# Performance work log

Hardware: AMD Instinct MI355X
Metric: run time of the kernel (lower is better)

Reference implementation:

```python
import jax, jax.numpy as jnp
import numpy as np

NEG = jnp.float32(-1e9)


def setup_inputs() -> dict:
    key = jax.random.key(0)
    ks = jax.random.split(key, 8)
    B, S, D = 8, 2048, 1024
    scale = 1.0 / np.sqrt(D)
    return {
        "xQ": jax.random.normal(ks[0], (B, S, D), jnp.float32),
        "xK": jax.random.normal(ks[1], (B, S, D), jnp.float32),
        "xV": jax.random.normal(ks[2], (B, S, D), jnp.float32),
        "padding_mask": jax.random.randint(ks[3], (B, S), 0, 2, jnp.int32),
        "casual_mask": jnp.ones((B, S), jnp.int32),
        "W_q": jax.random.normal(ks[4], (D, D), jnp.float32) * scale,
        "b_q": jnp.zeros((D,), jnp.float32),
        "W_k": jax.random.normal(ks[5], (D, D), jnp.float32) * scale,
        "b_k": jnp.zeros((D,), jnp.float32),
        "W_v": jax.random.normal(ks[6], (D, D), jnp.float32) * scale,
        "b_v": jnp.zeros((D,), jnp.float32),
    }


def reference(xQ, xK, xV, padding_mask, casual_mask, W_q, b_q, W_k, b_k, W_v, b_v):
    # Linear projections (torch nn.Linear: x @ W.T + b)
    Q = jnp.einsum('bsd,ed->bse', xQ, W_q) + b_q
    K = jnp.einsum('bsd,ed->bse', xK, W_k) + b_k
    V = jnp.einsum('bsd,ed->bse', xV, W_v) + b_v

    # Raw logits (note: original code applies NO 1/sqrt(dk) scaling)
    QKT = jnp.einsum('bqd,bkd->bqk', Q, K)  # [B, Sq, Sk]

    # Additive padding mask: -1e9 on padded key positions
    pad = jnp.where(padding_mask[:, None, :] == 0, NEG, jnp.float32(0.0))
    # Additive causal mask: -1e9 above the diagonal
    Sq, Sk = QKT.shape[1], QKT.shape[2]
    caus = jnp.where(
        jnp.tril(jnp.ones((Sq, Sk), dtype=bool)), jnp.float32(0.0), NEG
    )[None, :, :]
    QKT = QKT + pad + caus

    S = jax.nn.softmax(QKT, axis=-1)
    return jnp.einsum('bqk,bkd->bqd', S, V)
```

## Files before the change

### kernel.cpp

```cpp
#include <hip/hip_runtime.h>

typedef __attribute__((ext_vector_type(4))) float f4;
typedef __attribute__((ext_vector_type(4))) float f32x4;
typedef _Float16 half8 __attribute__((ext_vector_type(8)));

#define DEVI static __device__ __forceinline__

DEVI void gload_lds16(const void* g, void* l) {
  __builtin_amdgcn_global_load_lds(
      (const __attribute__((address_space(1))) void*)g,
      (__attribute__((address_space(3))) void*)l, 16, 0, 0);
}

DEVI int xcd_swz(int id, int n) {
  int q = n >> 3, r = n & 7;
  int x = id & 7, c = id >> 3;
  return (x < r ? x * (q + 1) : r * (q + 1) + (x - r) * q) + c;
}

#define FENCED_BARRIER()                \
  __builtin_amdgcn_sched_barrier(0);    \
  __builtin_amdgcn_s_barrier();         \
  __builtin_amdgcn_sched_barrier(0);

#define SWZ(kgv, rowv) ((((kgv) ^ ((rowv) >> 1)) & 3) * 8)

__global__ __launch_bounds__(256) void cvt_plain(const float* __restrict__ X,
                                                 _Float16* __restrict__ H,
                                                 int n4) {
  int i = blockIdx.x * 256 + threadIdx.x;
  const int stride = gridDim.x * 256;
  typedef _Float16 half4v __attribute__((ext_vector_type(4)));
  for (; i < n4; i += stride) {
    f4 x = ((const f4*)X)[i];
    half4v h;
#pragma unroll
    for (int j = 0; j < 4; ++j) h[j] = (_Float16)x[j];
    ((half4v*)H)[i] = h;
  }
}

__global__ __launch_bounds__(256) void cvt_split(const float* __restrict__ X,
                                                 _Float16* __restrict__ H,
                                                 _Float16* __restrict__ L,
                                                 int n4) {
  int i = blockIdx.x * 256 + threadIdx.x;
  const int stride = gridDim.x * 256;
  typedef _Float16 half4v __attribute__((ext_vector_type(4)));
  for (; i < n4; i += stride) {
    f4 x = ((const f4*)X)[i];
    half4v h, l;
#pragma unroll
    for (int j = 0; j < 4; ++j) {
      h[j] = (_Float16)x[j];
      l[j] = (_Float16)(x[j] - (float)h[j]);
    }
    ((half4v*)H)[i] = h;
    ((half4v*)L)[i] = l;
  }
}

DEVI void acc_zero44(f32x4 (&acc)[4][4]) {
#pragma unroll
  for (int i = 0; i < 4; ++i)
#pragma unroll
    for (int j = 0; j < 4; ++j) acc[i][j] = (f32x4)0.0f;
}
DEVI void acc_zero42(f32x4 (&acc)[4][2]) {
#pragma unroll
  for (int i = 0; i < 4; ++i)
#pragma unroll
    for (int j = 0; j < 2; ++j) acc[i][j] = (f32x4)0.0f;
}

template <int WSPLIT, int OUTMODE>
__global__ __launch_bounds__(512, 4) void proj3(
    const _Float16* __restrict__ X, const _Float16* __restrict__ Wh,
    const _Float16* __restrict__ Wl, const float* __restrict__ bias,
    _Float16* __restrict__ OutHi, _Float16* __restrict__ OutLo,
    _Float16* __restrict__ VtOut) {
  extern __shared__ _Float16 lds[];
  constexpr int ACH = 128 * 32;
  constexpr int BCH = 128 * 32;
  constexpr int CHUNK = ACH + BCH * (1 + WSPLIT);
  const int id = xcd_swz(blockIdx.x, gridDim.x);
  const int m0 = (id >> 3) * 128, n0 = (id & 7) * 128;
  const _Float16* A0 = X + (size_t)m0 * 1024;
  const _Float16* B0 = Wh + (size_t)n0 * 1024;
  const _Float16* B1 = Wl + (size_t)n0 * 1024;
  const int tid = threadIdx.x;
  const int w = tid >> 6, lane = tid & 63;
  const int wm = w >> 2, wn = w & 3;
  const int r16 = lane & 15, kg = lane >> 4;
  f32x4 acc[4][2];
  acc_zero42(acc);

  auto STAGE = [&](int t, int buf) {
    _Float16* base = lds + buf * CHUNK;
    int row = tid >> 2, c = tid & 3;
    int cs = (c ^ (row >> 1)) & 3;
    size_t src = (size_t)row * 1024 + t * 32 + cs * 8;
    gload_lds16(A0 + src, base + tid * 8);
    gload_lds16(B0 + src, base + ACH + tid * 8);
    if (WSPLIT) gload_lds16(B1 + src, base + ACH + BCH + tid * 8);
  };
  auto COMPUTE = [&](int buf) {
    const _Float16* la = lds + buf * CHUNK;
    const _Float16* lb = la + ACH;
    half8 a[4], b0f[2], b1f[2];
#pragma unroll
    for (int mi = 0; mi < 4; ++mi) {
      int row = wm * 64 + mi * 16 + r16;
      a[mi] = *(const half8*)(la + row * 32 + SWZ(kg, row));
    }
#pragma unroll
    for (int ni = 0; ni < 2; ++ni) {
      int row = wn * 32 + ni * 16 + r16;
      int off = row * 32 + SWZ(kg, row);
      b0f[ni] = *(const half8*)(lb + off);
      if (WSPLIT) b1f[ni] = *(const half8*)(lb + BCH + off);
    }
    __builtin_amdgcn_s_setprio(1);
#pragma unroll
    for (int mi = 0; mi < 4; ++mi)
#pragma unroll
      for (int ni = 0; ni < 2; ++ni) {
        acc[mi][ni] = __builtin_amdgcn_mfma_f32_16x16x32_f16(
            a[mi], b0f[ni], acc[mi][ni], 0, 0, 0);
        if (WSPLIT)
          acc[mi][ni] = __builtin_amdgcn_mfma_f32_16x16x32_f16(
              a[mi], b1f[ni], acc[mi][ni], 0, 0, 0);
      }
    __builtin_amdgcn_s_setprio(0);
  };

  const int NS = 32;
  STAGE(0, 0);
  STAGE(1, 1);
  int tt = 0;
  for (; tt < NS - 1; ++tt) {
    if constexpr (WSPLIT)
      asm volatile("s_waitcnt vmcnt(3)" ::: "memory");
    else
      asm volatile("s_waitcnt vmcnt(2)" ::: "memory");
    FENCED_BARRIER();
    if (tt + 2 < NS) STAGE(tt + 2, (tt + 2) % 3);
    COMPUTE(tt % 3);
  }
  asm volatile("s_waitcnt vmcnt(0)" ::: "memory");
  FENCED_BARRIER();
  COMPUTE(tt % 3);

  float bcol[2];
#pragma unroll
  for (int ni = 0; ni < 2; ++ni) bcol[ni] = bias[n0 + wn * 32 + ni * 16 + r16];

  if (OUTMODE != 2) {
#pragma unroll
    for (int mi = 0; mi < 4; ++mi) {
      int row = m0 + wm * 64 + mi * 16 + kg * 4;
#pragma unroll
      for (int ni = 0; ni < 2; ++ni) {
        int col = n0 + wn * 32 + ni * 16 + r16;
#pragma unroll
        for (int j = 0; j < 4; ++j) {
          float v = acc[mi][ni][j] + bcol[ni];
          _Float16 h = (_Float16)v;
          OutHi[(size_t)(row + j) * 1024 + col] = h;
          if (OUTMODE == 0)
            OutLo[(size_t)(row + j) * 1024 + col] = (_Float16)(v - (float)h);
        }
      }
    }
  } else {
    __syncthreads();
    _Float16(*T)[128] = (_Float16(*)[128])lds;
#pragma unroll
    for (int mi = 0; mi < 4; ++mi) {
      int ml = wm * 64 + mi * 16 + kg * 4;
#pragma unroll
      for (int ni = 0; ni < 2; ++ni) {
        int nl = wn * 32 + ni * 16 + r16;
#pragma unroll
        for (int j = 0; j < 4; ++j)
          T[nl][ml + j] = (_Float16)(acc[mi][ni][j] + bcol[ni]);
      }
    }
    __syncthreads();
    const int b = m0 >> 11;
    const int s0 = m0 & 2047;
#pragma unroll
    for (int r = 0; r < 4; ++r) {
      int flat = tid + r * 512;
      int n = flat >> 4, c = flat & 15;
      half8 v = *(const half8*)&T[n][c * 8];
      *(half8*)(VtOut + (size_t)b * (1024 * 2048) + (size_t)(n0 + n) * 2048 +
                s0 + c * 8) = v;
    }
  }
}

template <int WSPLIT, int OUTMODE>
__global__ __launch_bounds__(512, 2) void proj_fused(
    const float* __restrict__ X, const _Float16* __restrict__ Wh,
    const _Float16* __restrict__ Wl, const float* __restrict__ bias,
    _Float16* __restrict__ OutHi, _Float16* __restrict__ OutLo,
    _Float16* __restrict__ VtOut) {
  extern __shared__ _Float16 lds[];
  constexpr int ACH = 256 * 32;
  constexpr int BCH = 128 * 32;
  constexpr int CHUNK = ACH + BCH * (1 + WSPLIT);
  const int id = xcd_swz(blockIdx.x, gridDim.x);
  const int m0 = (id >> 3) * 256, n0 = (id & 7) * 128;
  const float* A = X + (size_t)m0 * 1024;
  const _Float16* B0 = Wh + (size_t)n0 * 1024;
  const _Float16* B1 = Wl + (size_t)n0 * 1024;
  const int tid = threadIdx.x;
  const int w = tid >> 6, lane = tid & 63;
  const int wm = w >> 1, wn = w & 1;
  const int r16 = lane & 15, kg = lane >> 4;
  f32x4 acc[4][4];
  acc_zero44(acc);
  f4 ra[4];

  auto ALOAD = [&](int t) {
#pragma unroll
    for (int j = 0; j < 2; ++j) {
      int g = tid + j * 512;
      int row = g >> 2, c = g & 3;
      const float* src = A + (size_t)row * 1024 + t * 32 + c * 8;
      ra[2 * j] = *(const f4*)src;
      ra[2 * j + 1] = *(const f4*)(src + 4);
    }
  };
  auto AWRITE = [&](int buf) {
    _Float16* ab = lds + buf * CHUNK;
#pragma unroll
    for (int j = 0; j < 2; ++j) {
      int g = tid + j * 512;
      int row = g >> 2, c = g & 3;
      half8 h;
#pragma unroll
      for (int e = 0; e < 4; ++e) {
        h[e] = (_Float16)ra[2 * j][e];
        h[e + 4] = (_Float16)ra[2 * j + 1][e];
      }
      *(half8*)(ab + (size_t)row * 32 + SWZ(c, row)) = h;
    }
  };
  auto WLOAD = [&](int t, int buf) {
    _Float16* bb = lds + buf * CHUNK + ACH;
    int row = tid >> 2, c = tid & 3;
    int cs = (c ^ (row >> 1)) & 3;
    gload_lds16(B0 + (size_t)row * 1024 + t * 32 + cs * 8, bb + tid * 8);
    if (WSPLIT)
      gload_lds16(B1 + (size_t)row * 1024 + t * 32 + cs * 8,
                  bb + BCH + tid * 8);
  };
  auto COMPUTE = [&](int buf) {
    const _Float16* la = lds + buf * CHUNK;
    const _Float16* lb = la + ACH;
    half8 a[4], b0f[4], b1f[4];
#pragma unroll
    for (int mi = 0; mi < 4; ++mi) {
      int row = wm * 64 + mi * 16 + r16;
      a[mi] = *(const half8*)(la + row * 32 + SWZ(kg, row));
    }
#pragma unroll
    for (int ni = 0; ni < 4; ++ni) {
      int row = wn * 64 + ni * 16 + r16;
      int off = row * 32 + SWZ(kg, row);
      b0f[ni] = *(const half8*)(lb + off);
      if (WSPLIT) b1f[ni] = *(const half8*)(lb + BCH + off);
    }
    __builtin_amdgcn_s_setprio(1);
#pragma unroll
    for (int mi = 0; mi < 4; ++mi)
#pragma unroll
      for (int ni = 0; ni < 4; ++ni) {
        acc[mi][ni] = __builtin_amdgcn_mfma_f32_16x16x32_f16(
            a[mi], b0f[ni], acc[mi][ni], 0, 0, 0);
        if (WSPLIT)
          acc[mi][ni] = __builtin_amdgcn_mfma_f32_16x16x32_f16(
              a[mi], b1f[ni], acc[mi][ni], 0, 0, 0);
      }
    __builtin_amdgcn_s_setprio(0);
  };

  const int NS = 32;
  WLOAD(0, 0);
  ALOAD(0);
  asm volatile("s_waitcnt vmcnt(0)" ::: "memory");
  __builtin_amdgcn_sched_barrier(0);
  AWRITE(0);
  asm volatile("s_waitcnt lgkmcnt(0)" ::: "memory");
  FENCED_BARRIER();
  for (int t = 0; t < NS; ++t) {
    if (t + 1 < NS) {
      WLOAD(t + 1, (t + 1) & 1);
      ALOAD(t + 1);
    }
    COMPUTE(t & 1);
    if (t + 1 < NS) {
      asm volatile("s_waitcnt vmcnt(0)" ::: "memory");
      __builtin_amdgcn_sched_barrier(0);
      AWRITE((t + 1) & 1);
      asm volatile("s_waitcnt lgkmcnt(0)" ::: "memory");
      FENCED_BARRIER();
    }
  }

  float bcol[4];
#pragma unroll
  for (int ni = 0; ni < 4; ++ni) bcol[ni] = bias[n0 + wn * 64 + ni * 16 + r16];

  if (OUTMODE != 2) {
#pragma unroll
    for (int mi = 0; mi < 4; ++mi) {
      int row = m0 + wm * 64 + mi * 16 + kg * 4;
#pragma unroll
      for (int ni = 0; ni < 4; ++ni) {
        int col = n0 + wn * 64 + ni * 16 + r16;
#pragma unroll
        for (int j = 0; j < 4; ++j) {
          float v = acc[mi][ni][j] + bcol[ni];
          _Float16 h = (_Float16)v;
          OutHi[(size_t)(row + j) * 1024 + col] = h;
          if (OUTMODE == 0)
            OutLo[(size_t)(row + j) * 1024 + col] = (_Float16)(v - (float)h);
        }
      }
    }
  } else {
    __syncthreads();
    _Float16(*T)[256] = (_Float16(*)[256])lds;
#pragma unroll
    for (int mi = 0; mi < 4; ++mi) {
      int ml = wm * 64 + mi * 16 + kg * 4;
#pragma unroll
      for (int ni = 0; ni < 4; ++ni) {
        int nl = wn * 64 + ni * 16 + r16;
#pragma unroll
        for (int j = 0; j < 4; ++j)
          T[nl][ml + j] = (_Float16)(acc[mi][ni][j] + bcol[ni]);
      }
    }
    __syncthreads();
    const int b = m0 >> 11;
    const int s0 = m0 & 2047;
#pragma unroll
    for (int r = 0; r < 8; ++r) {
      int flat = tid + r * 512;
      int n = flat >> 5, c = flat & 31;
      half8 v = *(const half8*)&T[n][c * 8];
      *(half8*)(VtOut + (size_t)b * (1024 * 2048) + (size_t)(n0 + n) * 2048 +
                s0 + c * 8) = v;
    }
  }
}

__global__ __launch_bounds__(512, 4) void qk_eng(
    const _Float16* __restrict__ Qh, const _Float16* __restrict__ Ql,
    const _Float16* __restrict__ Kh, const int* __restrict__ pad,
    float* __restrict__ Lg, int bbase) {
  extern __shared__ _Float16 lds[];
  constexpr int CHUNK = 12288;
  const int id = xcd_swz(blockIdx.x, gridDim.x);
  const int y = id / 144;
  int t = id % 144;
  int g4 = 0, base = 0;
  while (t >= base + (g4 + 1) * 4) { base += (g4 + 1) * 4; ++g4; }
  const int rem = t - base;
  const int qt = g4 * 4 + rem / (g4 + 1);
  const int kt = rem % (g4 + 1);
  const int b = bbase + y;
  const size_t boff = (size_t)b * (2048 * 1024);
  const _Float16* A0 = Qh + boff + (size_t)(qt * 64) * 1024;
  const _Float16* A1 = Ql + boff + (size_t)(qt * 64) * 1024;
  const _Float16* B0 = Kh + boff + (size_t)(kt * 256) * 1024;
  const int tid = threadIdx.x;
  const int w = tid >> 6, lane = tid & 63;
  const int r16 = lane & 15, kg = lane >> 4;
  const int wn = w;
  f32x4 acc[4][2];
  acc_zero42(acc);

  auto STAGE = [&](int t_, int buf) {
    _Float16* base_ = lds + buf * CHUNK;
    {
      int g = tid & 255;
      int row = g >> 2, c = g & 3;
      int cs = (c ^ (row >> 1)) & 3;
      const _Float16* src = (tid < 256) ? A0 : A1;
      _Float16* dst = base_ + ((tid < 256) ? 0 : 2048);
      gload_lds16(src + (size_t)row * 1024 + t_ * 32 + cs * 8, dst + g * 8);
    }
#pragma unroll
    for (int j = 0; j < 2; ++j) {
      int g = tid + j * 512;
      int row = g >> 2, c = g & 3;
      int cs = (c ^ (row >> 1)) & 3;
      gload_lds16(B0 + (size_t)row * 1024 + t_ * 32 + cs * 8,
                  base_ + 4096 + g * 8);
    }
  };
  auto COMPUTE = [&](int buf) {
    const _Float16* la = lds + buf * CHUNK;
    half8 a0[4], a1[4], bf[2];
#pragma unroll
    for (int mi = 0; mi < 4; ++mi) {
      int row = mi * 16 + r16;
      int off = row * 32 + SWZ(kg, row);
      a0[mi] = *(const half8*)(la + off);
      a1[mi] = *(const half8*)(la + 2048 + off);
    }
#pragma unroll
    for (int ni = 0; ni < 2; ++ni) {
      int row = wn * 32 + ni * 16 + r16;
      bf[ni] = *(const half8*)(la + 4096 + row * 32 + SWZ(kg, row));
    }
    __builtin_amdgcn_s_setprio(1);
#pragma unroll
    for (int mi = 0; mi < 4; ++mi)
#pragma unroll
      for (int ni = 0; ni < 2; ++ni) {
        acc[mi][ni] = __builtin_amdgcn_mfma_f32_16x16x32_f16(
            a0[mi], bf[ni], acc[mi][ni], 0, 0, 0);
        acc[mi][ni] = __builtin_amdgcn_mfma_f32_16x16x32_f16(
            a1[mi], bf[ni], acc[mi][ni], 0, 0, 0);
      }
    __builtin_amdgcn_s_setprio(0);
  };

  const int NS = 32;
  STAGE(0, 0);
  STAGE(1, 1);
  int tt = 0;
  for (; tt < NS - 1; ++tt) {
    asm volatile("s_waitcnt vmcnt(3)" ::: "memory");
    FENCED_BARRIER();
    if (tt + 2 < NS) STAGE(tt + 2, (tt + 2) % 3);
    COMPUTE(tt % 3);
  }
  asm volatile("s_waitcnt vmcnt(0)" ::: "memory");
  FENCED_BARRIER();
  COMPUTE(tt % 3);

  float* L = Lg + (size_t)y * (2048 * 2048);
  const int* pb = pad + (size_t)b * 2048;
#pragma unroll
  for (int ni = 0; ni < 2; ++ni) {
    int col = kt * 256 + wn * 32 + ni * 16 + r16;
    const float padd = (pb[col] == 0) ? -1.0e9f : 0.0f;
#pragma unroll
    for (int mi = 0; mi < 4; ++mi) {
      int row = qt * 64 + mi * 16 + kg * 4;
#pragma unroll
      for (int j = 0; j < 4; ++j)
        L[(size_t)(row + j) * 2048 + col] = acc[mi][ni][j] + padd;
    }
  }
}

__global__ __launch_bounds__(512, 4) void pv_eng(
    const float* __restrict__ Lg, const _Float16* __restrict__ Vt,
    float* __restrict__ Out, int bbase, int ntiles) {
  extern __shared__ _Float16 lds[];
  constexpr int CHUNK = 8192;
  const int g0 = xcd_swz(blockIdx.x, gridDim.x);
  const int tid = threadIdx.x;
  const int w = tid >> 6, lane = tid & 63;
  const int wm = w >> 2, wn = w & 3;
  const int r16 = lane & 15, kg = lane >> 4;

  for (int half = 0; half < 2; ++half) {
    const int idt = half ? (ntiles - 1 - g0) : g0;
    const int y = idt >> 7;
    const int qt = (idt & 127) >> 3, nt = idt & 7;
    const int b = bbase + y;
    const _Float16* P = (const _Float16*)(Lg + (size_t)y * (2048 * 2048));
    const _Float16* A0 = P + (size_t)(qt * 128) * 4096;
    const _Float16* B0 =
        Vt + (size_t)b * (1024 * 2048) + (size_t)(nt * 128) * 2048;
    const int NS = (qt + 1) * 4;
    f32x4 acc[4][2];
    acc_zero42(acc);

    auto STAGE = [&](int t_, int buf) {
      _Float16* base_ = lds + buf * CHUNK;
      int row = tid >> 2, c = tid & 3;
      int cs = (c ^ (row >> 1)) & 3;
      gload_lds16(A0 + (size_t)row * 4096 + t_ * 32 + cs * 8, base_ + tid * 8);
      gload_lds16(B0 + (size_t)row * 2048 + t_ * 32 + cs * 8,
                  base_ + 4096 + tid * 8);
    };
    auto COMPUTE = [&](int buf) {
      const _Float16* la = lds + buf * CHUNK;
      half8 a[4], bf[2];
#pragma unroll
      for (int mi = 0; mi < 4; ++mi) {
        int row = wm * 64 + mi * 16 + r16;
        a[mi] = *(const half8*)(la + row * 32 + SWZ(kg, row));
      }
#pragma unroll
      for (int ni = 0; ni < 2; ++ni) {
        int row = wn * 32 + ni * 16 + r16;
        bf[ni] = *(const half8*)(la + 4096 + row * 32 + SWZ(kg, row));
      }
      __builtin_amdgcn_s_setprio(1);
#pragma unroll
      for (int mi = 0; mi < 4; ++mi)
#pragma unroll
        for (int ni = 0; ni < 2; ++ni)
          acc[mi][ni] = __builtin_amdgcn_mfma_f32_16x16x32_f16(
              a[mi], bf[ni], acc[mi][ni], 0, 0, 0);
      __builtin_amdgcn_s_setprio(0);
    };

    STAGE(0, 0);
    STAGE(1, 1);
    int tt = 0;
    for (; tt < NS - 1; ++tt) {
      asm volatile("s_waitcnt vmcnt(2)" ::: "memory");
      FENCED_BARRIER();
      if (tt + 2 < NS) STAGE(tt + 2, (tt + 2) % 3);
      COMPUTE(tt % 3);
    }
    asm volatile("s_waitcnt vmcnt(0)" ::: "memory");
    FENCED_BARRIER();
    COMPUTE(tt % 3);

#pragma unroll
    for (int mi = 0; mi < 4; ++mi) {
      int row = qt * 128 + wm * 64 + mi * 16 + kg * 4;
#pragma unroll
      for (int ni = 0; ni < 2; ++ni) {
        int col = nt * 128 + wn * 32 + ni * 16 + r16;
#pragma unroll
        for (int j = 0; j < 4; ++j)
          Out[(size_t)(b * 2048 + row + j) * 1024 + col] = acc[mi][ni][j];
      }
    }
    if (half == 0) {
      asm volatile("s_waitcnt vmcnt(0) lgkmcnt(0)" ::: "memory");
      FENCED_BARRIER();
    }
  }
}

__global__ __launch_bounds__(256) void softmax_kernel(float* __restrict__ Lg,
                                                      int bbase) {
  const int q = blockIdx.x;
  const int y = blockIdx.y;
  const int tid = threadIdx.x;
  float* row = Lg + (size_t)y * (2048 * 2048) + (size_t)q * 2048;
  _Float16* prow = (_Float16*)row;
  const int kend = ((q >> 8) + 1) << 8;
  float v[8];
  int nv = 0;
  float mx = -3.0e38f;
  for (int k = tid; k <= q; k += 256) {
    float l = row[k];
    v[nv++] = l;
    mx = fmaxf(mx, l);
  }
  __shared__ float red[4];
  for (int o = 32; o; o >>= 1) mx = fmaxf(mx, __shfl_xor(mx, o));
  if ((tid & 63) == 0) red[tid >> 6] = mx;
  __syncthreads();
  mx = fmaxf(fmaxf(red[0], red[1]), fmaxf(red[2], red[3]));
  __syncthreads();
  float s = 0.f;
  for (int i = 0; i < nv; ++i) s += expf(v[i] - mx);
  for (int o = 32; o; o >>= 1) s += __shfl_xor(s, o);
  if ((tid & 63) == 0) red[tid >> 6] = s;
  __syncthreads();
  s = red[0] + red[1] + red[2] + red[3];
  const float inv = 1.0f / s;
  int i = 0;
  for (int k = tid; k <= q; k += 256) {
    prow[k] = (_Float16)(expf(v[i] - mx) * inv);
    ++i;
  }
  for (int k = q + 1 + tid; k < kend; k += 256) prow[k] = (_Float16)0.0f;
}

__global__ __launch_bounds__(512) void fix_f(const int* __restrict__ pad,
                                             int* __restrict__ fb) {
  const int b = threadIdx.x >> 6, k = threadIdx.x & 63;
  unsigned long long m = __ballot(pad[b * 2048 + k] != 0);
  if (k == 0) fb[b] = m ? (__ffsll((long long)m) - 1) : 64;
}

__global__ __launch_bounds__(256) void fix_qrow2(
    const float* __restrict__ xQ, const float* __restrict__ Wq,
    const float* __restrict__ bq, const int* __restrict__ fb,
    float* __restrict__ Qrow) {
  const int b = blockIdx.y;
  const int f = fb[b];
  const int tid = threadIdx.x;
  const int e = blockIdx.x * 16 + (tid >> 4);
  const int l16 = tid & 15;
  __shared__ float xq[1024];
  for (int q = 0; q < f; ++q) {
    *(f4*)&xq[tid * 4] = ((const f4*)(xQ + (size_t)(b * 2048 + q) * 1024))[tid];
    __syncthreads();
    float a = 0.f;
#pragma unroll
    for (int it = 0; it < 16; ++it) {
      int d = l16 * 4 + it * 64;
      f4 ww = *(const f4*)(Wq + (size_t)e * 1024 + d);
      a += xq[d] * ww[0] + xq[d + 1] * ww[1] + xq[d + 2] * ww[2] +
           xq[d + 3] * ww[3];
    }
    for (int o = 8; o; o >>= 1) a += __shfl_xor(a, o);
    if (l16 == 0) Qrow[((size_t)b * 64 + q) * 1024 + e] = a + bq[e];
    __syncthreads();
  }
}

__global__ __launch_bounds__(256) void fix_qb0(const float* __restrict__ bk,
                                               const int* __restrict__ fb,
                                               const float* __restrict__ Qrow,
                                               float* __restrict__ qb0) {
  const int q = blockIdx.x, b = blockIdx.y;
  if (q >= fb[b]) return;
  const int tid = threadIdx.x;
  const float* qr = Qrow + ((size_t)b * 64 + q) * 1024;
  float p = 0.f;
  for (int e = tid; e < 1024; e += 256) p += qr[e] * bk[e];
  __shared__ float red[4];
  for (int o = 32; o; o >>= 1) p += __shfl_xor(p, o);
  if ((tid & 63) == 0) red[tid >> 6] = p;
  __syncthreads();
  if (tid == 0) qb0[b * 64 + q] = red[0] + red[1] + red[2] + red[3];
}

__global__ __launch_bounds__(256) void fix_g2(const float* __restrict__ Wk,
                                              const int* __restrict__ fb,
                                              const float* __restrict__ Qrow,
                                              float* __restrict__ Gpart) {
  const int b = blockIdx.y;
  const int f = fb[b];
  const int tid = threadIdx.x;
  const int ddblk = blockIdx.x & 3, es = blockIdx.x >> 2;
  const int dd = ddblk * 256 + tid;
  __shared__ float qc[128];
  for (int q = 0; q < f; ++q) {
    if (tid < 32)
      *(f4*)&qc[tid * 4] =
          ((const f4*)(Qrow + ((size_t)b * 64 + q) * 1024 + es * 128))[tid];
    __syncthreads();
    float g = 0.f;
    for (int e = 0; e < 128; ++e)
      g += qc[e] * Wk[(size_t)(es * 128 + e) * 1024 + dd];
    Gpart[(((size_t)es * 8 + b) * 64 + q) * 1024 + dd] = g;
    __syncthreads();
  }
}

__global__ __launch_bounds__(256) void fix_logit2(
    const float* __restrict__ xK, const int* __restrict__ pad,
    const int* __restrict__ fb, const float* __restrict__ Gpart,
    const float* __restrict__ qb0, float* __restrict__ lrow) {
  const int b = blockIdx.y;
  const int f = fb[b];
  const int tid = threadIdx.x;
  const int k = blockIdx.x * 16 + (tid >> 4);
  const int l16 = tid & 15;
  __shared__ float Gs[1024];
  for (int q = 0; q < f; ++q) {
    f4 s = (f4)0.0f;
#pragma unroll
    for (int es = 0; es < 8; ++es)
      s += ((const f4*)(Gpart + (((size_t)es * 8 + b) * 64 + q) * 1024))[tid];
    *(f4*)&Gs[tid * 4] = s;
    __syncthreads();
    float a = 0.f;
#pragma unroll
    for (int it = 0; it < 16; ++it) {
      int d = l16 * 4 + it * 64;
      f4 x = *(const f4*)(xK + (size_t)(b * 2048 + k) * 1024 + d);
      a += x[0] * Gs[d] + x[1] * Gs[d + 1] + x[2] * Gs[d + 2] +
           x[3] * Gs[d + 3];
    }
    for (int o = 8; o; o >>= 1) a += __shfl_xor(a, o);
    if (l16 == 0) {
      float l = a + qb0[b * 64 + q];
      if (pad[b * 2048 + k] == 0) l += -1.0e9f;
      if (k > q) l += -1.0e9f;
      lrow[((size_t)b * 64 + q) * 2048 + k] = l;
    }
    __syncthreads();
  }
}

__global__ __launch_bounds__(256) void fix_sm(const int* __restrict__ fb,
                                              float* __restrict__ lrow,
                                              float* __restrict__ srow) {
  const int q = blockIdx.x, b = blockIdx.y;
  if (q >= fb[b]) return;
  const int tid = threadIdx.x;
  float* row = lrow + ((size_t)b * 64 + q) * 2048;
  float v[8];
  float mx = -3.0e38f;
#pragma unroll
  for (int i = 0; i < 8; ++i) {
    v[i] = row[tid + i * 256];
    mx = fmaxf(mx, v[i]);
  }
  __shared__ float red[4];
  for (int o = 32; o; o >>= 1) mx = fmaxf(mx, __shfl_xor(mx, o));
  if ((tid & 63) == 0) red[tid >> 6] = mx;
  __syncthreads();
  mx = fmaxf(fmaxf(red[0], red[1]), fmaxf(red[2], red[3]));
  __syncthreads();
  float s = 0.f;
#pragma unroll
  for (int i = 0; i < 8; ++i) {
    v[i] = expf(v[i] - mx);
    s += v[i];
  }
#pragma unroll
  for (int i = 0; i < 8; ++i) row[tid + i * 256] = v[i];
  for (int o = 32; o; o >>= 1) s += __shfl_xor(s, o);
  if ((tid & 63) == 0) red[tid >> 6] = s;
  __syncthreads();
  if (tid == 0) srow[b * 64 + q] = red[0] + red[1] + red[2] + red[3];
}

__global__ __launch_bounds__(256) void fix_pv2(
    const _Float16* __restrict__ Vt, const int* __restrict__ fb,
    const float* __restrict__ lrow, const float* __restrict__ srow,
    float* __restrict__ Out) {
  const int b = blockIdx.y;
  const int f = fb[b];
  const int tid = threadIdx.x;
  const int d = blockIdx.x * 16 + (tid >> 4);
  const int l16 = tid & 15;
  __shared__ float ps[2048];
  for (int q = 0; q < f; ++q) {
    const f4* src = (const f4*)(lrow + ((size_t)b * 64 + q) * 2048);
    *(f4*)&ps[tid * 8] = src[tid * 2];
    *(f4*)&ps[tid * 8 + 4] = src[tid * 2 + 1];
    __syncthreads();
    float o = 0.f;
#pragma unroll
    for (int it = 0; it < 16; ++it) {
      int k = l16 * 8 + it * 128;
      half8 vv = *(const half8*)(Vt + (size_t)b * (1024 * 2048) +
                                 (size_t)d * 2048 + k);
      o += (float)vv[0] * ps[k] + (float)vv[1] * ps[k + 1] +
           (float)vv[2] * ps[k + 2] + (float)vv[3] * ps[k + 3] +
           (float)vv[4] * ps[k + 4] + (float)vv[5] * ps[k + 5] +
           (float)vv[6] * ps[k + 6] + (float)vv[7] * ps[k + 7];
    }
    for (int of = 8; of; of >>= 1) o += __shfl_xor(o, of);
    if (l16 == 0)
      Out[(size_t)(b * 2048 + q) * 1024 + d] = o * (1.0f / srow[b * 64 + q]);
    __syncthreads();
  }
}

extern "C" void kernel_launch(void* const* d_in, const int* in_sizes, int n_in,
                              void* d_out, int out_size, void* d_ws,
                              size_t ws_size, hipStream_t stream) {
  const float* xQ = (const float*)d_in[0];
  const float* xK = (const float*)d_in[1];
  const float* xV = (const float*)d_in[2];
  const int* pad = (const int*)d_in[3];
  const float* Wq = (const float*)d_in[5];
  const float* bq = (const float*)d_in[6];
  const float* Wk = (const float*)d_in[7];
  const float* bk = (const float*)d_in[8];
  const float* Wv = (const float*)d_in[9];
  const float* bv = (const float*)d_in[10];
  float* Out = (float*)d_out;

  const size_t MB = (size_t)1 << 20;
  char* wsb = (char*)d_ws;
  _Float16* Qh = (_Float16*)(wsb);
  _Float16* Ql = (_Float16*)(wsb + 32 * MB);
  _Float16* Kh = (_Float16*)(wsb + 64 * MB);
  _Float16* Vt = (_Float16*)(wsb + 96 * MB);
  float* Lg = (float*)(wsb + 128 * MB);

  size_t avail = (ws_size > 128 * MB) ? ws_size - 128 * MB : 0;
  int G = (int)(avail / (16 * MB));
  if (G > 8) G = 8;
  if (G < 1) G = 1;

  const int SM_P1 = 73728;
  const int SM_P0 = 49152;
  const int SM_F = 65536;
  const int SM_QK = 73728;
  const int SM_PV = 49152;
  (void)hipFuncSetAttribute((const void*)&proj3<1, 0>,
                            hipFuncAttributeMaxDynamicSharedMemorySize, SM_P1);
  (void)hipFuncSetAttribute((const void*)&proj3<1, 1>,
                            hipFuncAttributeMaxDynamicSharedMemorySize, SM_P1);
  (void)hipFuncSetAttribute((const void*)&proj3<0, 2>,
                            hipFuncAttributeMaxDynamicSharedMemorySize, SM_P0);
  (void)hipFuncSetAttribute((const void*)&proj_fused<1, 0>,
                            hipFuncAttributeMaxDynamicSharedMemorySize, SM_F);
  (void)hipFuncSetAttribute((const void*)&proj_fused<1, 1>,
                            hipFuncAttributeMaxDynamicSharedMemorySize, SM_F);
  (void)hipFuncSetAttribute((const void*)&proj_fused<0, 2>,
                            hipFuncAttributeMaxDynamicSharedMemorySize, SM_F);
  (void)hipFuncSetAttribute((const void*)&qk_eng,
                            hipFuncAttributeMaxDynamicSharedMemorySize, SM_QK);
  (void)hipFuncSetAttribute((const void*)&pv_eng,
                            hipFuncAttributeMaxDynamicSharedMemorySize, SM_PV);

  dim3 blk(256), eblk(512);

  if (ws_size >= 165 * MB) {
    {
      _Float16* sX = (_Float16*)(wsb);
      _Float16* sW = (_Float16*)(wsb + 32 * MB);
      cvt_plain<<<dim3(2048), blk, 0, stream>>>(xV, sX, 4194304);
      cvt_plain<<<dim3(1024), blk, 0, stream>>>(Wv, sW, 262144);
      proj3<0, 2><<<dim3(1024), eblk, SM_P0, stream>>>(sX, sW, sW, bv, nullptr,
                                                       nullptr, Vt);
    }
    {
      _Float16* sX = (_Float16*)(wsb);
      _Float16* sWh = (_Float16*)(wsb + 32 * MB);
      _Float16* sWl = (_Float16*)(wsb + 34 * MB);
      cvt_plain<<<dim3(2048), blk, 0, stream>>>(xK, sX, 4194304);
      cvt_split<<<dim3(1024), blk, 0, stream>>>(Wk, sWh, sWl, 262144);
      proj3<1, 1><<<dim3(1024), eblk, SM_P1, stream>>>(sX, sWh, sWl, bk, Kh,
                                                       nullptr, nullptr);
    }
    {
      _Float16* sX = (_Float16*)(wsb + 128 * MB);
      _Float16* sWh = (_Float16*)(wsb + 160 * MB);
      _Float16* sWl = (_Float16*)(wsb + 162 * MB);
      cvt_plain<<<dim3(2048), blk, 0, stream>>>(xQ, sX, 4194304);
      cvt_split<<<dim3(1024), blk, 0, stream>>>(Wq, sWh, sWl, 262144);
      proj3<1, 0><<<dim3(1024), eblk, SM_P1, stream>>>(sX, sWh, sWl, bq, Qh,
                                                       Ql, nullptr);
    }
  } else {
    _Float16* Wqh = (_Float16*)(wsb + 128 * MB);
    _Float16* Wql = (_Float16*)(wsb + 130 * MB);
    _Float16* Wkh = (_Float16*)(wsb + 132 * MB);
    _Float16* Wkl = (_Float16*)(wsb + 134 * MB);
    _Float16* Wvh = (_Float16*)(wsb + 136 * MB);
    cvt_split<<<dim3(1024), blk, 0, stream>>>(Wq, Wqh, Wql, 262144);
    cvt_split<<<dim3(1024), blk, 0, stream>>>(Wk, Wkh, Wkl, 262144);
    cvt_plain<<<dim3(1024), blk, 0, stream>>>(Wv, Wvh, 262144);
    proj_fused<0, 2><<<dim3(512), eblk, SM_F, stream>>>(xV, Wvh, Wvh, bv,
                                                        nullptr, nullptr, Vt);
    proj_fused<1, 1><<<dim3(512), eblk, SM_F, stream>>>(xK, Wkh, Wkl, bk, Kh,
                                                        nullptr, nullptr);
    proj_fused<1, 0><<<dim3(512), eblk, SM_F, stream>>>(xQ, Wqh, Wql, bq, Qh,
                                                        Ql, nullptr);
  }

  for (int bbase = 0; bbase < 8; bbase += G) {
    int nb = (8 - bbase < G) ? (8 - bbase) : G;
    qk_eng<<<dim3(144 * nb), eblk, SM_QK, stream>>>(Qh, Ql, Kh, pad, Lg,
                                                    bbase);
    softmax_kernel<<<dim3(2048, nb), blk, 0, stream>>>(Lg, bbase);
    pv_eng<<<dim3(64 * nb), eblk, SM_PV, stream>>>(Lg, Vt, Out, bbase,
                                                   128 * nb);
  }

  int* fb = (int*)(wsb);
  float* qb0 = (float*)(wsb + 4 * 1024);
  float* srow = (float*)(wsb + 8 * 1024);
  float* Qrow = (float*)(wsb + 1 * MB);
  float* Gpart = (float*)(wsb + 4 * MB);
  float* lrow = (float*)(wsb + 20 * MB);

  fix_f<<<dim3(1), dim3(512), 0, stream>>>(pad, fb);
  fix_qrow2<<<dim3(64, 8), blk, 0, stream>>>(xQ, Wq, bq, fb, Qrow);
  fix_qb0<<<dim3(64, 8), blk, 0, stream>>>(bk, fb, Qrow, qb0);
  fix_g2<<<dim3(32, 8), blk, 0, stream>>>(Wk, fb, Qrow, Gpart);
  fix_logit2<<<dim3(128, 8), blk, 0, stream>>>(xK, pad, fb, Gpart, qb0, lrow);
  fix_sm<<<dim3(64, 8), blk, 0, stream>>>(fb, lrow, srow);
  fix_pv2<<<dim3(64, 8), blk, 0, stream>>>(Vt, fb, lrow, srow, Out);
}
```

Baseline: 496.1 us.

## Use 4-wave blocks with 64x64 per-wave tiles in projection, QK and PV GEMMs

Switches proj3, qk_eng and pv_eng from 512-thread blocks with 64x32 per-wave tiles to 256-thread blocks where each wave computes a 64x64 tile. Each thread now issues twice as many global-to-LDS loads per stage, and the vmcnt waits are scaled to match. The aim is more MFMA work per LDS fragment load and fewer waves per block, at the cost of higher register pressure and lower occupancy. Batch chunking for the attention loop is also rebalanced so chunks have near-equal sizes.

```diff
diff --git a/kernel.cpp b/kernel.cpp
--- a/kernel.cpp
+++ b/kernel.cpp
@@ -66,15 +66,9 @@
 #pragma unroll
     for (int j = 0; j < 4; ++j) acc[i][j] = (f32x4)0.0f;
 }
-DEVI void acc_zero42(f32x4 (&acc)[4][2]) {
-#pragma unroll
-  for (int i = 0; i < 4; ++i)
-#pragma unroll
-    for (int j = 0; j < 2; ++j) acc[i][j] = (f32x4)0.0f;
-}
 
 template <int WSPLIT, int OUTMODE>
-__global__ __launch_bounds__(512, 4) void proj3(
+__global__ __launch_bounds__(256, 2) void proj3(
     const _Float16* __restrict__ X, const _Float16* __restrict__ Wh,
     const _Float16* __restrict__ Wl, const float* __restrict__ bias,
     _Float16* __restrict__ OutHi, _Float16* __restrict__ OutLo,
@@ -90,32 +84,36 @@
   const _Float16* B1 = Wl + (size_t)n0 * 1024;
   const int tid = threadIdx.x;
   const int w = tid >> 6, lane = tid & 63;
-  const int wm = w >> 2, wn = w & 3;
+  const int wm = w >> 1, wn = w & 1;
   const int r16 = lane & 15, kg = lane >> 4;
-  f32x4 acc[4][2];
-  acc_zero42(acc);
+  f32x4 acc[4][4];
+  acc_zero44(acc);
 
   auto STAGE = [&](int t, int buf) {
     _Float16* base = lds + buf * CHUNK;
-    int row = tid >> 2, c = tid & 3;
-    int cs = (c ^ (row >> 1)) & 3;
-    size_t src = (size_t)row * 1024 + t * 32 + cs * 8;
-    gload_lds16(A0 + src, base + tid * 8);
-    gload_lds16(B0 + src, base + ACH + tid * 8);
-    if (WSPLIT) gload_lds16(B1 + src, base + ACH + BCH + tid * 8);
+#pragma unroll
+    for (int j = 0; j < 2; ++j) {
+      int g = tid + j * 256;
+      int row = g >> 2, c = g & 3;
+      int cs = (c ^ (row >> 1)) & 3;
+      size_t src = (size_t)row * 1024 + t * 32 + cs * 8;
+      gload_lds16(A0 + src, base + g * 8);
+      gload_lds16(B0 + src, base + ACH + g * 8);
+      if (WSPLIT) gload_lds16(B1 + src, base + ACH + BCH + g * 8);
+    }
   };
   auto COMPUTE = [&](int buf) {
     const _Float16* la = lds + buf * CHUNK;
     const _Float16* lb = la + ACH;
-    half8 a[4], b0f[2], b1f[2];
+    half8 a[4], b0f[4], b1f[4];
 #pragma unroll
     for (int mi = 0; mi < 4; ++mi) {
       int row = wm * 64 + mi * 16 + r16;
       a[mi] = *(const half8*)(la + row * 32 + SWZ(kg, row));
     }
 #pragma unroll
-    for (int ni = 0; ni < 2; ++ni) {
-      int row = wn * 32 + ni * 16 + r16;
+    for (int ni = 0; ni < 4; ++ni) {
+      int row = wn * 64 + ni * 16 + r16;
       int off = row * 32 + SWZ(kg, row);
       b0f[ni] = *(const half8*)(lb + off);
       if (WSPLIT) b1f[ni] = *(const half8*)(lb + BCH + off);
@@ -124,7 +122,7 @@
 #pragma unroll
     for (int mi = 0; mi < 4; ++mi)
 #pragma unroll
-      for (int ni = 0; ni < 2; ++ni) {
+      for (int ni = 0; ni < 4; ++ni) {
         acc[mi][ni] = __builtin_amdgcn_mfma_f32_16x16x32_f16(
             a[mi], b0f[ni], acc[mi][ni], 0, 0, 0);
         if (WSPLIT)
@@ -140,9 +138,9 @@
   int tt = 0;
   for (; tt < NS - 1; ++tt) {
     if constexpr (WSPLIT)
-      asm volatile("s_waitcnt vmcnt(3)" ::: "memory");
+      asm volatile("s_waitcnt vmcnt(6)" ::: "memory");
     else
-      asm volatile("s_waitcnt vmcnt(2)" ::: "memory");
+      asm volatile("s_waitcnt vmcnt(4)" ::: "memory");
     FENCED_BARRIER();
     if (tt + 2 < NS) STAGE(tt + 2, (tt + 2) % 3);
     COMPUTE(tt % 3);
@@ -151,17 +149,17 @@
   FENCED_BARRIER();
   COMPUTE(tt % 3);
 
-  float bcol[2];
-#pragma unroll
-  for (int ni = 0; ni < 2; ++ni) bcol[ni] = bias[n0 + wn * 32 + ni * 16 + r16];
+  float bcol[4];
+#pragma unroll
+  for (int ni = 0; ni < 4; ++ni) bcol[ni] = bias[n0 + wn * 64 + ni * 16 + r16];
 
   if (OUTMODE != 2) {
 #pragma unroll
     for (int mi = 0; mi < 4; ++mi) {
       int row = m0 + wm * 64 + mi * 16 + kg * 4;
 #pragma unroll
-      for (int ni = 0; ni < 2; ++ni) {
-        int col = n0 + wn * 32 + ni * 16 + r16;
+      for (int ni = 0; ni < 4; ++ni) {
+        int col = n0 + wn * 64 + ni * 16 + r16;
 #pragma unroll
         for (int j = 0; j < 4; ++j) {
           float v = acc[mi][ni][j] + bcol[ni];
@@ -179,8 +177,8 @@
     for (int mi = 0; mi < 4; ++mi) {
       int ml = wm * 64 + mi * 16 + kg * 4;
 #pragma unroll
-      for (int ni = 0; ni < 2; ++ni) {
-        int nl = wn * 32 + ni * 16 + r16;
+      for (int ni = 0; ni < 4; ++ni) {
+        int nl = wn * 64 + ni * 16 + r16;
 #pragma unroll
         for (int j = 0; j < 4; ++j)
           T[nl][ml + j] = (_Float16)(acc[mi][ni][j] + bcol[ni]);
@@ -190,8 +188,8 @@
     const int b = m0 >> 11;
     const int s0 = m0 & 2047;
 #pragma unroll
-    for (int r = 0; r < 4; ++r) {
-      int flat = tid + r * 512;
+    for (int r = 0; r < 8; ++r) {
+      int flat = tid + r * 256;
       int n = flat >> 4, c = flat & 15;
       half8 v = *(const half8*)&T[n][c * 8];
       *(half8*)(VtOut + (size_t)b * (1024 * 2048) + (size_t)(n0 + n) * 2048 +
@@ -359,7 +357,7 @@
   }
 }
 
-__global__ __launch_bounds__(512, 4) void qk_eng(
+__global__ __launch_bounds__(256, 2) void qk_eng(
     const _Float16* __restrict__ Qh, const _Float16* __restrict__ Ql,
     const _Float16* __restrict__ Kh, const int* __restrict__ pad,
     float* __restrict__ Lg, int bbase) {
@@ -382,22 +380,21 @@
   const int w = tid >> 6, lane = tid & 63;
   const int r16 = lane & 15, kg = lane >> 4;
   const int wn = w;
-  f32x4 acc[4][2];
-  acc_zero42(acc);
+  f32x4 acc[4][4];
+  acc_zero44(acc);
 
   auto STAGE = [&](int t_, int buf) {
     _Float16* base_ = lds + buf * CHUNK;
     {
-      int g = tid & 255;
-      int row = g >> 2, c = g & 3;
+      int row = tid >> 2, c = tid & 3;
       int cs = (c ^ (row >> 1)) & 3;
-      const _Float16* src = (tid < 256) ? A0 : A1;
-      _Float16* dst = base_ + ((tid < 256) ? 0 : 2048);
-      gload_lds16(src + (size_t)row * 1024 + t_ * 32 + cs * 8, dst + g * 8);
-    }
-#pragma unroll
-    for (int j = 0; j < 2; ++j) {
-      int g = tid + j * 512;
+      size_t src = (size_t)row * 1024 + t_ * 32 + cs * 8;
+      gload_lds16(A0 + src, base_ + tid * 8);
+      gload_lds16(A1 + src, base_ + 2048 + tid * 8);
+    }
+#pragma unroll
+    for (int j = 0; j < 4; ++j) {
+      int g = tid + j * 256;
       int row = g >> 2, c = g & 3;
       int cs = (c ^ (row >> 1)) & 3;
       gload_lds16(B0 + (size_t)row * 1024 + t_ * 32 + cs * 8,
@@ -406,7 +403,7 @@
   };
   auto COMPUTE = [&](int buf) {
     const _Float16* la = lds + buf * CHUNK;
-    half8 a0[4], a1[4], bf[2];
+    half8 a0[4], a1[4], bf[4];
 #pragma unroll
     for (int mi = 0; mi < 4; ++mi) {
       int row = mi * 16 + r16;
@@ -415,15 +412,15 @@
       a1[mi] = *(const half8*)(la + 2048 + off);
     }
 #pragma unroll
-    for (int ni = 0; ni < 2; ++ni) {
-      int row = wn * 32 + ni * 16 + r16;
+    for (int ni = 0; ni < 4; ++ni) {
+      int row = wn * 64 + ni * 16 + r16;
       bf[ni] = *(const half8*)(la + 4096 + row * 32 + SWZ(kg, row));
     }
     __builtin_amdgcn_s_setprio(1);
 #pragma unroll
     for (int mi = 0; mi < 4; ++mi)
 #pragma unroll
-      for (int ni = 0; ni < 2; ++ni) {
+      for (int ni = 0; ni < 4; ++ni) {
         acc[mi][ni] = __builtin_amdgcn_mfma_f32_16x16x32_f16(
             a0[mi], bf[ni], acc[mi][ni], 0, 0, 0);
         acc[mi][ni] = __builtin_amdgcn_mfma_f32_16x16x32_f16(
@@ -437,7 +434,7 @@
   STAGE(1, 1);
   int tt = 0;
   for (; tt < NS - 1; ++tt) {
-    asm volatile("s_waitcnt vmcnt(3)" ::: "memory");
+    asm volatile("s_waitcnt vmcnt(6)" ::: "memory");
     FENCED_BARRIER();
     if (tt + 2 < NS) STAGE(tt + 2, (tt + 2) % 3);
     COMPUTE(tt % 3);
@@ -449,8 +446,8 @@
   float* L = Lg + (size_t)y * (2048 * 2048);
   const int* pb = pad + (size_t)b * 2048;
 #pragma unroll
-  for (int ni = 0; ni < 2; ++ni) {
-    int col = kt * 256 + wn * 32 + ni * 16 + r16;
+  for (int ni = 0; ni < 4; ++ni) {
+    int col = kt * 256 + wn * 64 + ni * 16 + r16;
     const float padd = (pb[col] == 0) ? -1.0e9f : 0.0f;
 #pragma unroll
     for (int mi = 0; mi < 4; ++mi) {
@@ -462,7 +459,7 @@
   }
 }
 
-__global__ __launch_bounds__(512, 4) void pv_eng(
+__global__ __launch_bounds__(256, 3) void pv_eng(
     const float* __restrict__ Lg, const _Float16* __restrict__ Vt,
     float* __restrict__ Out, int bbase, int ntiles) {
   extern __shared__ _Float16 lds[];
@@ -470,7 +467,7 @@
   const int g0 = xcd_swz(blockIdx.x, gridDim.x);
   const int tid = threadIdx.x;
   const int w = tid >> 6, lane = tid & 63;
-  const int wm = w >> 2, wn = w & 3;
+  const int wm = w >> 1, wn = w & 1;
   const int r16 = lane & 15, kg = lane >> 4;
 
   for (int half = 0; half < 2; ++half) {
@@ -483,35 +480,39 @@
     const _Float16* B0 =
         Vt + (size_t)b * (1024 * 2048) + (size_t)(nt * 128) * 2048;
     const int NS = (qt + 1) * 4;
-    f32x4 acc[4][2];
-    acc_zero42(acc);
+    f32x4 acc[4][4];
+    acc_zero44(acc);
 
     auto STAGE = [&](int t_, int buf) {
       _Float16* base_ = lds + buf * CHUNK;
-      int row = tid >> 2, c = tid & 3;
-      int cs = (c ^ (row >> 1)) & 3;
-      gload_lds16(A0 + (size_t)row * 4096 + t_ * 32 + cs * 8, base_ + tid * 8);
-      gload_lds16(B0 + (size_t)row * 2048 + t_ * 32 + cs * 8,
-                  base_ + 4096 + tid * 8);
+#pragma unroll
+      for (int j = 0; j < 2; ++j) {
+        int g = tid + j * 256;
+        int row = g >> 2, c = g & 3;
+        int cs = (c ^ (row >> 1)) & 3;
+        gload_lds16(A0 + (size_t)row * 4096 + t_ * 32 + cs * 8, base_ + g * 8);
+        gload_lds16(B0 + (size_t)row * 2048 + t_ * 32 + cs * 8,
+                    base_ + 4096 + g * 8);
+      }
     };
     auto COMPUTE = [&](int buf) {
       const _Float16* la = lds + buf * CHUNK;
-      half8 a[4], bf[2];
+      half8 a[4], bf[4];
 #pragma unroll
       for (int mi = 0; mi < 4; ++mi) {
         int row = wm * 64 + mi * 16 + r16;
         a[mi] = *(const half8*)(la + row * 32 + SWZ(kg, row));
       }
 #pragma unroll
-      for (int ni = 0; ni < 2; ++ni) {
-        int row = wn * 32 + ni * 16 + r16;
+      for (int ni = 0; ni < 4; ++ni) {
+        int row = wn * 64 + ni * 16 + r16;
         bf[ni] = *(const half8*)(la + 4096 + row * 32 + SWZ(kg, row));
       }
       __builtin_amdgcn_s_setprio(1);
 #pragma unroll
       for (int mi = 0; mi < 4; ++mi)
 #pragma unroll
-        for (int ni = 0; ni < 2; ++ni)
+        for (int ni = 0; ni < 4; ++ni)
           acc[mi][ni] = __builtin_amdgcn_mfma_f32_16x16x32_f16(
               a[mi], bf[ni], acc[mi][ni], 0, 0, 0);
       __builtin_amdgcn_s_setprio(0);
@@ -521,7 +522,7 @@
     STAGE(1, 1);
     int tt = 0;
     for (; tt < NS - 1; ++tt) {
-      asm volatile("s_waitcnt vmcnt(2)" ::: "memory");
+      asm volatile("s_waitcnt vmcnt(4)" ::: "memory");
       FENCED_BARRIER();
       if (tt + 2 < NS) STAGE(tt + 2, (tt + 2) % 3);
       COMPUTE(tt % 3);
@@ -534,8 +535,8 @@
     for (int mi = 0; mi < 4; ++mi) {
       int row = qt * 128 + wm * 64 + mi * 16 + kg * 4;
 #pragma unroll
-      for (int ni = 0; ni < 2; ++ni) {
-        int col = nt * 128 + wn * 32 + ni * 16 + r16;
+      for (int ni = 0; ni < 4; ++ni) {
+        int col = nt * 128 + wn * 64 + ni * 16 + r16;
 #pragma unroll
         for (int j = 0; j < 4; ++j)
           Out[(size_t)(b * 2048 + row + j) * 1024 + col] = acc[mi][ni][j];
@@ -789,9 +790,11 @@
   int G = (int)(avail / (16 * MB));
   if (G > 8) G = 8;
   if (G < 1) G = 1;
+  int nchunks = (8 + G - 1) / G;
+  int base_nb = 8 / nchunks, extra = 8 % nchunks;
 
   const int SM_P1 = 73728;
-  const int SM_P0 = 49152;
+  const int SM_P0 = 73728;
   const int SM_F = 65536;
   const int SM_QK = 73728;
   const int SM_PV = 49152;
@@ -820,8 +823,8 @@
       _Float16* sW = (_Float16*)(wsb + 32 * MB);
       cvt_plain<<<dim3(2048), blk, 0, stream>>>(xV, sX, 4194304);
       cvt_plain<<<dim3(1024), blk, 0, stream>>>(Wv, sW, 262144);
-      proj3<0, 2><<<dim3(1024), eblk, SM_P0, stream>>>(sX, sW, sW, bv, nullptr,
-                                                       nullptr, Vt);
+      proj3<0, 2><<<dim3(1024), blk, SM_P0, stream>>>(sX, sW, sW, bv, nullptr,
+                                                      nullptr, Vt);
     }
     {
       _Float16* sX = (_Float16*)(wsb);
@@ -829,8 +832,8 @@
       _Float16* sWl = (_Float16*)(wsb + 34 * MB);
       cvt_plain<<<dim3(2048), blk, 0, stream>>>(xK, sX, 4194304);
       cvt_split<<<dim3(1024), blk, 0, stream>>>(Wk, sWh, sWl, 262144);
-      proj3<1, 1><<<dim3(1024), eblk, SM_P1, stream>>>(sX, sWh, sWl, bk, Kh,
-                                                       nullptr, nullptr);
+      proj3<1, 1><<<dim3(1024), blk, SM_P1, stream>>>(sX, sWh, sWl, bk, Kh,
+                                                      nullptr, nullptr);
     }
     {
       _Float16* sX = (_Float16*)(wsb + 128 * MB);
@@ -838,8 +841,8 @@
       _Float16* sWl = (_Float16*)(wsb + 162 * MB);
       cvt_plain<<<dim3(2048), blk, 0, stream>>>(xQ, sX, 4194304);
       cvt_split<<<dim3(1024), blk, 0, stream>>>(Wq, sWh, sWl, 262144);
-      proj3<1, 0><<<dim3(1024), eblk, SM_P1, stream>>>(sX, sWh, sWl, bq, Qh,
-                                                       Ql, nullptr);
+      proj3<1, 0><<<dim3(1024), blk, SM_P1, stream>>>(sX, sWh, sWl, bq, Qh,
+                                                      Ql, nullptr);
     }
   } else {
     _Float16* Wqh = (_Float16*)(wsb + 128 * MB);
@@ -858,13 +861,15 @@
                                                         Ql, nullptr);
   }
 
-  for (int bbase = 0; bbase < 8; bbase += G) {
-    int nb = (8 - bbase < G) ? (8 - bbase) : G;
-    qk_eng<<<dim3(144 * nb), eblk, SM_QK, stream>>>(Qh, Ql, Kh, pad, Lg,
-                                                    bbase);
+  int bbase = 0;
+  for (int c = 0; c < nchunks; ++c) {
+    int nb = base_nb + (c < extra ? 1 : 0);
+    if (nb <= 0) break;
+    qk_eng<<<dim3(144 * nb), blk, SM_QK, stream>>>(Qh, Ql, Kh, pad, Lg, bbase);
     softmax_kernel<<<dim3(2048, nb), blk, 0, stream>>>(Lg, bbase);
-    pv_eng<<<dim3(64 * nb), eblk, SM_PV, stream>>>(Lg, Vt, Out, bbase,
-                                                   128 * nb);
+    pv_eng<<<dim3(64 * nb), blk, SM_PV, stream>>>(Lg, Vt, Out, bbase,
+                                                  128 * nb);
+    bbase += nb;
   }
 
   int* fb = (int*)(wsb);
```

Result: no change. 499.0 us (+0.6%).
